# Kernel optimization log

Measured on AMD Instinct MI355X. Metric: run time of the kernel, lower is better.

## Reference

```python
import jax, jax.numpy as jnp
import numpy as np

B, C, H, W = 8, 256, 128, 128
CQ = C // 8


def setup_inputs() -> dict:
    key = jax.random.key(0)
    ks = jax.random.split(key, 8)
    s = 1.0 / np.sqrt(C)
    return {
        "x": jax.random.normal(ks[0], (B, C, H, W), dtype=jnp.float32),
        "wq": jax.random.normal(ks[1], (CQ, C), dtype=jnp.float32) * s,
        "bq": jax.random.normal(ks[2], (CQ,), dtype=jnp.float32) * 0.01,
        "wk": jax.random.normal(ks[3], (CQ, C), dtype=jnp.float32) * s,
        "bk": jax.random.normal(ks[4], (CQ,), dtype=jnp.float32) * 0.01,
        "wv": jax.random.normal(ks[5], (C, C), dtype=jnp.float32) * s,
        "bv": jax.random.normal(ks[6], (C,), dtype=jnp.float32) * 0.01,
        "gamma": jax.random.normal(ks[7], (1,), dtype=jnp.float32) * 0.1,
    }


def reference(x, wq, bq, wk, bk, wv, bv, gamma):
    b, c, h, w = x.shape
    # 1x1 convs == channel matmuls
    q = jnp.einsum("oc,bchw->bohw", wq, x) + bq[None, :, None, None]  # [B,Cq,H,W]
    k = jnp.einsum("oc,bchw->bohw", wk, x) + bk[None, :, None, None]  # [B,Cq,H,W]
    v = jnp.einsum("oc,bchw->bohw", wv, x) + bv[None, :, None, None]  # [B,C,H,W]

    # column (height) scores: energy_H[b,i,w,j] = <k[:, i, w], q[:, j, w]>, -inf on i==j
    e_h = jnp.einsum("bciw,bcjw->biwj", k, q)  # [B,H,W,H]
    diag = jnp.eye(h, dtype=bool)[:, None, :]  # [H,1,H] -> masks i==j
    e_h = jnp.where(diag[None], -jnp.inf, e_h)

    # row (width) scores: energy_W[b,h,i,j] = <k[:, h, i], q[:, h, j]>
    e_w = jnp.einsum("bchi,bchj->bhij", k, q)  # [B,H,W,W]

    # joint softmax over concatenated H+W scores (axis 3), as in the torch code
    att = jax.nn.softmax(jnp.concatenate([e_h, e_w], axis=3), axis=3)
    a_h, a_w = att[..., :h], att[..., h:]

    out_h = jnp.einsum("bciw,biwj->bcjw", v, a_h)  # aggregate along column
    out_w = jnp.einsum("bchi,bhij->bchj", v, a_w)  # aggregate along row
    return gamma * (out_h + out_w) + x
```

## Files before the change

### kernel.cpp

```cpp
#include <hip/hip_runtime.h>
#include <math.h>

#define C_   256
#define CQ_  32
#define H_   128
#define W_   128
#define HW_  (H_ * W_)
#define OC_  320

typedef __attribute__((ext_vector_type(8))) short  s8v;
typedef __attribute__((ext_vector_type(4))) float  f4v;
typedef __attribute__((ext_vector_type(8))) unsigned short u8v;
typedef __attribute__((ext_vector_type(4))) unsigned short u4v;

__device__ inline unsigned short f2bf(float f) {
    unsigned int u = __float_as_uint(f);
    unsigned int r = (u + 0x7fffu + ((u >> 16) & 1u)) >> 16;
    return (unsigned short)r;
}
__device__ inline float bfu(unsigned short u) {
    return __uint_as_float((unsigned int)u << 16);
}

__global__ __launch_bounds__(256) void k_wconv(
    const float* __restrict__ wq, const float* __restrict__ wk,
    const float* __restrict__ wv, unsigned short* __restrict__ Wb)
{
    int idx4 = blockIdx.x * 256 + threadIdx.x;
    int e = idx4 * 4;
    int oc = e >> 8, k = e & 255;
    const float* src;
    if (oc < 32)      src = wq + (size_t)oc * C_ + k;
    else if (oc < 64) src = wk + (size_t)(oc - 32) * C_ + k;
    else              src = wv + (size_t)(oc - 64) * C_ + k;
    float4 v = *(const float4*)src;
    u4v o;
    o[0] = f2bf(v.x); o[1] = f2bf(v.y); o[2] = f2bf(v.z); o[3] = f2bf(v.w);
    *(u4v*)(Wb + e) = o;
}

__global__ __launch_bounds__(256) void k_qkv(
    const float* __restrict__ x, const unsigned short* __restrict__ Wb,
    const float* __restrict__ bq, const float* __restrict__ bk,
    const float* __restrict__ bv,
    unsigned short* __restrict__ qkv, int b0)
{
    __shared__ __align__(16) unsigned short Wl[64][264];
    __shared__ __align__(16) unsigned int   Xp[32 * 132];
    const int t = threadIdx.x;
    const int lane = t & 63;
    const int wave = t >> 6;
    const int n0 = blockIdx.x * 128;
    const int ocblk = blockIdx.y * 64;
    const int bb = blockIdx.z;
    const float* xb = x + (size_t)(b0 + bb) * C_ * HW_;

    const int lg = lane >> 4;
    const int ll = lane & 15;
    const int n_w = wave * 32;

    const int kp8 = t >> 5;
    const int n4  = (t & 31) * 4;
    float4 ra[4], rb[4];

    #pragma unroll
    for (int p = 0; p < 4; ++p) {
        int krow = (p * 8 + kp8) * 2;
        ra[p] = *(const float4*)(xb + (size_t)krow * HW_ + n0 + n4);
        rb[p] = *(const float4*)(xb + (size_t)(krow + 1) * HW_ + n0 + n4);
    }

    #pragma unroll
    for (int q = 0; q < 8; ++q) {
        int chunk = t + q * 256;
        int row = chunk >> 5;
        int col = (chunk & 31) * 8;
        u8v w = *(const u8v*)(Wb + (size_t)(ocblk + row) * C_ + col);
        *(u8v*)&Wl[row][col] = w;
    }

    f4v acc[4][2];
    #pragma unroll
    for (int mr = 0; mr < 4; ++mr)
        #pragma unroll
        for (int nr = 0; nr < 2; ++nr)
            acc[mr][nr] = (f4v){0.f, 0.f, 0.f, 0.f};

    #pragma unroll
    for (int kc = 0; kc < 4; ++kc) {
        __syncthreads();
        #pragma unroll
        for (int p = 0; p < 4; ++p) {
            uint4 d;
            const float* af  = (const float*)&ra[p];
            const float* bf_ = (const float*)&rb[p];
            #pragma unroll
            for (int i = 0; i < 4; ++i) {
                unsigned int lo = (__float_as_uint(af[i])  + 0x8000u) >> 16;
                unsigned int hi = (__float_as_uint(bf_[i]) + 0x8000u) & 0xffff0000u;
                ((unsigned int*)&d)[i] = hi | lo;
            }
            *(uint4*)&Xp[(p * 8 + kp8) * 132 + n4] = d;
        }
        __syncthreads();
        if (kc < 3) {
            #pragma unroll
            for (int p = 0; p < 4; ++p) {
                int krow = (kc + 1) * 64 + (p * 8 + kp8) * 2;
                ra[p] = *(const float4*)(xb + (size_t)krow * HW_ + n0 + n4);
                rb[p] = *(const float4*)(xb + (size_t)(krow + 1) * HW_ + n0 + n4);
            }
        }
        #pragma unroll
        for (int ks = 0; ks < 2; ++ks) {
            s8v afr[4];
            #pragma unroll
            for (int mr = 0; mr < 4; ++mr)
                afr[mr] = *(const s8v*)&Wl[mr * 16 + ll][(kc * 2 + ks) * 32 + lg * 8];
            #pragma unroll
            for (int nr = 0; nr < 2; ++nr) {
                int4 bd;
                #pragma unroll
                for (int e2 = 0; e2 < 4; ++e2)
                    ((int*)&bd)[e2] =
                        Xp[(ks * 16 + lg * 4 + e2) * 132 + n_w + nr * 16 + ll];
                s8v bfr = *(s8v*)&bd;
                #pragma unroll
                for (int mr = 0; mr < 4; ++mr)
                    acc[mr][nr] = __builtin_amdgcn_mfma_f32_16x16x32_bf16(
                        afr[mr], bfr, acc[mr][nr], 0, 0, 0);
            }
        }
    }

    #pragma unroll
    for (int mr = 0; mr < 4; ++mr) {
        float bias[4];
        #pragma unroll
        for (int r = 0; r < 4; ++r) {
            int oc = ocblk + mr * 16 + lg * 4 + r;
            if (oc < 32)      bias[r] = bq[oc];
            else if (oc < 64) bias[r] = bk[oc - 32];
            else              bias[r] = bv[oc - 64];
        }
        #pragma unroll
        for (int nr = 0; nr < 2; ++nr) {
            int n = n0 + n_w + nr * 16 + ll;
            #pragma unroll
            for (int r = 0; r < 4; ++r) {
                int oc = ocblk + mr * 16 + lg * 4 + r;
                qkv[((size_t)bb * OC_ + oc) * HW_ + n] = f2bf(acc[mr][nr][r] + bias[r]);
            }
        }
    }
}

__global__ __launch_bounds__(256) void k_transpose_qkv(
    const unsigned short* __restrict__ qkv, unsigned short* __restrict__ qkv_t)
{
    __shared__ unsigned short tile[32][34];
    const int bb = blockIdx.z;
    const int oc = blockIdx.y;
    const int th = (blockIdx.x & 3) * 32;
    const int tw = (blockIdx.x >> 2) * 32;
    const unsigned short* src = qkv + ((size_t)bb * OC_ + oc) * HW_;
    #pragma unroll
    for (int r = 0; r < 4; ++r) {
        int h = threadIdx.y * 4 + r;
        tile[h][threadIdx.x] = src[(size_t)(th + h) * W_ + tw + threadIdx.x];
    }
    __syncthreads();
    unsigned short* dst = qkv_t + (size_t)bb * W_ * OC_ * H_;
    #pragma unroll
    for (int r = 0; r < 4; ++r) {
        int wl = threadIdx.y * 4 + r;
        dst[((size_t)(tw + wl) * OC_ + oc) * H_ + th + threadIdx.x] = tile[threadIdx.x][wl];
    }
}

__device__ inline void stage_KQ(const unsigned short* base, int cstride,
                                unsigned int* Ktp, unsigned int* Qp, int t)
{
    {
        int i = t & 127, half = t >> 7, c0 = half * 16;
        unsigned int kr[16];
        #pragma unroll
        for (int cc = 0; cc < 16; ++cc)
            kr[cc] = base[(size_t)(32 + c0 + cc) * cstride + i];
        uint4 d0, d1;
        #pragma unroll
        for (int e2 = 0; e2 < 4; ++e2)
            ((unsigned int*)&d0)[e2] = kr[2 * e2] | (kr[2 * e2 + 1] << 16);
        #pragma unroll
        for (int e2 = 0; e2 < 4; ++e2)
            ((unsigned int*)&d1)[e2] = kr[8 + 2 * e2] | (kr[9 + 2 * e2] << 16);
        *(uint4*)&Ktp[i * 20 + half * 8]     = d0;
        *(uint4*)&Ktp[i * 20 + half * 8 + 4] = d1;
    }
    {
        int c2 = t >> 4, j8 = (t & 15) * 8;
        u8v qa = *(const u8v*)(base + (size_t)(2 * c2) * cstride + j8);
        u8v qb = *(const u8v*)(base + (size_t)(2 * c2 + 1) * cstride + j8);
        uint4 e0, e1;
        #pragma unroll
        for (int e = 0; e < 4; ++e)
            ((unsigned int*)&e0)[e] =
                (unsigned int)qa[e] | ((unsigned int)qb[e] << 16);
        #pragma unroll
        for (int e = 0; e < 4; ++e)
            ((unsigned int*)&e1)[e] =
                (unsigned int)qa[4 + e] | ((unsigned int)qb[4 + e] << 16);
        *(uint4*)&Qp[c2 * 132 + j8]     = e0;
        *(uint4*)&Qp[c2 * 132 + j8 + 4] = e1;
    }
}

__device__ inline f4v eqk_mfma(const unsigned int* Ktp, const unsigned int* Qp,
                               int mr, int j, int lg, int ll)
{
    s8v afr = *(const s8v*)&Ktp[(mr * 16 + ll) * 20 + lg * 4];
    int4 bd;
    #pragma unroll
    for (int e2 = 0; e2 < 4; ++e2)
        ((int*)&bd)[e2] = Qp[(lg * 4 + e2) * 132 + j];
    s8v bfr = *(s8v*)&bd;
    return __builtin_amdgcn_mfma_f32_16x16x32_bf16(
        afr, bfr, (f4v){0.f, 0.f, 0.f, 0.f}, 0, 0, 0);
}

__global__ __launch_bounds__(256) void k_stats_h(
    const unsigned short* __restrict__ qkv_t,
    float* __restrict__ mh, float* __restrict__ sh)
{
    __shared__ __align__(16) unsigned int Ktp[128 * 20];
    __shared__ __align__(16) unsigned int Qp[16 * 132];
    const int t = threadIdx.x;
    const int beta = blockIdx.x;
    const int bb = blockIdx.y;
    const unsigned short* base = qkv_t + ((size_t)bb * W_ + beta) * OC_ * H_;
    stage_KQ(base, H_, Ktp, Qp, t);
    __syncthreads();

    const int lane = t & 63;
    const int wv = t >> 6;
    const int lg = lane >> 4;
    const int ll = lane & 15;

    #pragma unroll
    for (int ml = 0; ml < 2; ++ml) {
        const int mr = wv * 2 + ml;
        const int i0 = mr * 16 + lg * 4;
        f4v ef[8];
        #pragma unroll
        for (int nt = 0; nt < 8; ++nt) {
            f4v e = eqk_mfma(Ktp, Qp, mr, nt * 16 + ll, lg, ll);
            int j = nt * 16 + ll;
            #pragma unroll
            for (int r = 0; r < 4; ++r)
                if (i0 + r == j) e[r] = -INFINITY;
            ef[nt] = e;
        }
        #pragma unroll
        for (int r = 0; r < 4; ++r) {
            float mm = -INFINITY;
            #pragma unroll
            for (int nt = 0; nt < 8; ++nt) mm = fmaxf(mm, ef[nt][r]);
            #pragma unroll
            for (int s = 1; s < 16; s <<= 1) mm = fmaxf(mm, __shfl_xor(mm, s));
            float ss = 0.f;
            #pragma unroll
            for (int nt = 0; nt < 8; ++nt) ss += __expf(ef[nt][r] - mm);
            #pragma unroll
            for (int s = 1; s < 16; s <<= 1) ss += __shfl_xor(ss, s);
            if (ll == 0) {
                int i = i0 + r;
                mh[((size_t)bb * H_ + i) * W_ + beta] = mm;
                sh[((size_t)bb * H_ + i) * W_ + beta] = ss;
            }
        }
    }
}

__global__ __launch_bounds__(256) void k_stats_w(
    const unsigned short* __restrict__ qkv,
    float* __restrict__ mw, float* __restrict__ sw)
{
    __shared__ __align__(16) unsigned int Ktp[128 * 20];
    __shared__ __align__(16) unsigned int Qp[16 * 132];
    const int t = threadIdx.x;
    const int alpha = blockIdx.x;
    const int bb = blockIdx.y;
    const unsigned short* base = qkv + (size_t)bb * OC_ * HW_ + (size_t)alpha * W_;
    stage_KQ(base, HW_, Ktp, Qp, t);
    __syncthreads();

    const int lane = t & 63;
    const int wv = t >> 6;
    const int lg = lane >> 4;
    const int ll = lane & 15;

    #pragma unroll
    for (int ml = 0; ml < 2; ++ml) {
        const int mr = wv * 2 + ml;
        const int i0 = mr * 16 + lg * 4;
        f4v ef[8];
        #pragma unroll
        for (int nt = 0; nt < 8; ++nt)
            ef[nt] = eqk_mfma(Ktp, Qp, mr, nt * 16 + ll, lg, ll);
        #pragma unroll
        for (int r = 0; r < 4; ++r) {
            float mm = -INFINITY;
            #pragma unroll
            for (int nt = 0; nt < 8; ++nt) mm = fmaxf(mm, ef[nt][r]);
            #pragma unroll
            for (int s = 1; s < 16; s <<= 1) mm = fmaxf(mm, __shfl_xor(mm, s));
            float ss = 0.f;
            #pragma unroll
            for (int nt = 0; nt < 8; ++nt) ss += __expf(ef[nt][r] - mm);
            #pragma unroll
            for (int s = 1; s < 16; s <<= 1) ss += __shfl_xor(ss, s);
            if (ll == 0) {
                int i = i0 + r;
                mw[((size_t)bb * H_ + alpha) * W_ + i] = mm;
                sw[((size_t)bb * H_ + alpha) * W_ + i] = ss;
            }
        }
    }
}

__global__ __launch_bounds__(256) void k_prep(
    const float* __restrict__ mh, const float* __restrict__ sh,
    const float* __restrict__ mw, const float* __restrict__ sw,
    float* __restrict__ mc, float* __restrict__ dv,
    float* __restrict__ mct, float* __restrict__ dvt, int n)
{
    int idx = blockIdx.x * 256 + threadIdx.x;
    if (idx >= n) return;
    float m1 = mh[idx], s1 = sh[idx], m2 = mw[idx], s2 = sw[idx];
    float m = fmaxf(m1, m2);
    float d = 1.f / (s1 * __expf(m1 - m) + s2 * __expf(m2 - m));
    mc[idx] = m; dv[idx] = d;
    int q = idx & (W_ - 1);
    int p = (idx >> 7) & (H_ - 1);
    int b = idx >> 14;
    size_t tid = ((size_t)b * W_ + q) * H_ + p;
    mct[tid] = m; dvt[tid] = d;
}

__global__ __launch_bounds__(256) void k_outh(
    const unsigned short* __restrict__ qkv_t,
    const float* __restrict__ mct, const float* __restrict__ dvt,
    unsigned short* __restrict__ oh_t)
{
    __shared__ __align__(16) unsigned short Pt[128 * 128];
    __shared__ __align__(16) unsigned char  Ubuf[18688];
    __shared__ float mloc[128], dloc[128];
    unsigned int* Ktp = (unsigned int*)Ubuf;
    unsigned int* Qp  = (unsigned int*)(Ubuf + 10240);
    unsigned short* Vl = (unsigned short*)Ubuf;

    const int t = threadIdx.x;
    const int beta = blockIdx.x;
    const int bb = blockIdx.y;
    const unsigned short* base = qkv_t + ((size_t)bb * W_ + beta) * OC_ * H_;

    if (t < 128) {
        size_t sidx = ((size_t)bb * W_ + beta) * H_ + t;
        mloc[t] = mct[sidx];
        dloc[t] = dvt[sidx];
    }
    stage_KQ(base, H_, Ktp, Qp, t);
    __syncthreads();

    const int lane = t & 63;
    const int wv = t >> 6;
    const int lg = lane >> 4;
    const int ll = lane & 15;
    const int jq0 = wv * 32;

    #pragma unroll
    for (int mr = 0; mr < 8; ++mr) {
        const int i0 = mr * 16 + lg * 4;
        float mi[4], di[4];
        #pragma unroll
        for (int r = 0; r < 4; ++r) { mi[r] = mloc[i0 + r]; di[r] = dloc[i0 + r]; }
        #pragma unroll
        for (int nt = 0; nt < 2; ++nt) {
            int j = jq0 + nt * 16 + ll;
            f4v e = eqk_mfma(Ktp, Qp, mr, j, lg, ll);
            float p0 = (i0     == j) ? 0.f : __expf(e[0] - mi[0]) * di[0];
            float p1 = (i0 + 1 == j) ? 0.f : __expf(e[1] - mi[1]) * di[1];
            float p2 = (i0 + 2 == j) ? 0.f : __expf(e[2] - mi[2]) * di[2];
            float p3 = (i0 + 3 == j) ? 0.f : __expf(e[3] - mi[3]) * di[3];
            uint2 wd;
            wd.x = f2bf(p0) | ((unsigned int)f2bf(p1) << 16);
            wd.y = f2bf(p2) | ((unsigned int)f2bf(p3) << 16);
            int sidx = (j * 128 + i0) ^ ((j & 7) << 3);
            *(uint2*)&Pt[sidx] = wd;
        }
    }

    unsigned short* outbase = oh_t + ((size_t)bb * W_ + beta) * C_ * H_;

    for (int ch = 0; ch < 4; ++ch) {
        __syncthreads();
        const unsigned short* vsrc = base + (size_t)(64 + ch * 64) * H_;
        #pragma unroll
        for (int f = t; f < 1024; f += 256) {
            int c = f >> 4, i0 = (f & 15) * 8;
            u8v v = *(const u8v*)(vsrc + (size_t)c * H_ + i0);
            *(u8v*)&Vl[(c * 128 + i0) ^ ((c & 7) << 3)] = v;
        }
        __syncthreads();

        f4v acc[8];
        #pragma unroll
        for (int nt = 0; nt < 8; ++nt) acc[nt] = (f4v){0.f, 0.f, 0.f, 0.f};

        #pragma unroll
        for (int kk = 0; kk < 4; ++kk) {
            int crow = wv * 16 + ll;
            s8v afr = *(const s8v*)&Vl[(crow * 128 + kk * 32 + lg * 8) ^ ((crow & 7) << 3)];
            #pragma unroll
            for (int nt = 0; nt < 8; ++nt) {
                int j = nt * 16 + ll;
                s8v bfr = *(const s8v*)&Pt[(j * 128 + kk * 32 + lg * 8) ^ ((j & 7) << 3)];
                acc[nt] = __builtin_amdgcn_mfma_f32_16x16x32_bf16(afr, bfr, acc[nt], 0, 0, 0);
            }
        }
        #pragma unroll
        for (int nt = 0; nt < 8; ++nt) {
            int j = nt * 16 + ll;
            #pragma unroll
            for (int r = 0; r < 4; ++r) {
                int c = ch * 64 + wv * 16 + lg * 4 + r;
                outbase[(size_t)c * H_ + j] = f2bf(acc[nt][r]);
            }
        }
    }
}

__global__ __launch_bounds__(256) void k_outw(
    const unsigned short* __restrict__ qkv,
    const float* __restrict__ mc, const float* __restrict__ dv_,
    unsigned short* __restrict__ ow)
{
    __shared__ __align__(16) unsigned short Pt[128 * 128];
    __shared__ __align__(16) unsigned char  Ubuf[18688];
    __shared__ float mloc[128], dloc[128];
    unsigned int* Ktp = (unsigned int*)Ubuf;
    unsigned int* Qp  = (unsigned int*)(Ubuf + 10240);
    unsigned short* Vl = (unsigned short*)Ubuf;

    const int t = threadIdx.x;
    const int alpha = blockIdx.x;
    const int bb = blockIdx.y;
    const unsigned short* base = qkv + (size_t)bb * OC_ * HW_ + (size_t)alpha * W_;

    if (t < 128) {
        size_t sidx = ((size_t)bb * H_ + alpha) * W_ + t;
        mloc[t] = mc[sidx];
        dloc[t] = dv_[sidx];
    }
    stage_KQ(base, HW_, Ktp, Qp, t);
    __syncthreads();

    const int lane = t & 63;
    const int wv = t >> 6;
    const int lg = lane >> 4;
    const int ll = lane & 15;
    const int jq0 = wv * 32;

    #pragma unroll
    for (int mr = 0; mr < 8; ++mr) {
        const int i0 = mr * 16 + lg * 4;
        float mi[4], di[4];
        #pragma unroll
        for (int r = 0; r < 4; ++r) { mi[r] = mloc[i0 + r]; di[r] = dloc[i0 + r]; }
        #pragma unroll
        for (int nt = 0; nt < 2; ++nt) {
            int j = jq0 + nt * 16 + ll;
            f4v e = eqk_mfma(Ktp, Qp, mr, j, lg, ll);
            float p0 = __expf(e[0] - mi[0]) * di[0];
            float p1 = __expf(e[1] - mi[1]) * di[1];
            float p2 = __expf(e[2] - mi[2]) * di[2];
            float p3 = __expf(e[3] - mi[3]) * di[3];
            uint2 wd;
            wd.x = f2bf(p0) | ((unsigned int)f2bf(p1) << 16);
            wd.y = f2bf(p2) | ((unsigned int)f2bf(p3) << 16);
            int sidx = (j * 128 + i0) ^ ((j & 7) << 3);
            *(uint2*)&Pt[sidx] = wd;
        }
    }

    unsigned short* obase = ow + (size_t)bb * C_ * HW_ + (size_t)alpha * W_;

    for (int ch = 0; ch < 4; ++ch) {
        __syncthreads();
        const unsigned short* vsrc = base + (size_t)(64 + ch * 64) * HW_;
        #pragma unroll
        for (int f = t; f < 1024; f += 256) {
            int c = f >> 4, i0 = (f & 15) * 8;
            u8v v = *(const u8v*)(vsrc + (size_t)c * HW_ + i0);
            *(u8v*)&Vl[(c * 128 + i0) ^ ((c & 7) << 3)] = v;
        }
        __syncthreads();

        f4v acc[8];
        #pragma unroll
        for (int nt = 0; nt < 8; ++nt) acc[nt] = (f4v){0.f, 0.f, 0.f, 0.f};

        #pragma unroll
        for (int kk = 0; kk < 4; ++kk) {
            int crow = wv * 16 + ll;
            s8v afr = *(const s8v*)&Vl[(crow * 128 + kk * 32 + lg * 8) ^ ((crow & 7) << 3)];
            #pragma unroll
            for (int nt = 0; nt < 8; ++nt) {
                int j = nt * 16 + ll;
                s8v bfr = *(const s8v*)&Pt[(j * 128 + kk * 32 + lg * 8) ^ ((j & 7) << 3)];
                acc[nt] = __builtin_amdgcn_mfma_f32_16x16x32_bf16(afr, bfr, acc[nt], 0, 0, 0);
            }
        }
        #pragma unroll
        for (int nt = 0; nt < 8; ++nt) {
            int j = nt * 16 + ll;
            #pragma unroll
            for (int r = 0; r < 4; ++r) {
                int c = ch * 64 + wv * 16 + lg * 4 + r;
                obase[(size_t)c * HW_ + j] = f2bf(acc[nt][r]);
            }
        }
    }
}

__global__ __launch_bounds__(256) void k_combine(
    const unsigned short* __restrict__ oh_t, const unsigned short* __restrict__ ow,
    const float* __restrict__ x, const float* __restrict__ gamma_p,
    float* __restrict__ out, int b0)
{
    __shared__ float tile[32][33];
    const int bb = blockIdx.z;
    const int c = blockIdx.y;
    const int th = (blockIdx.x & 3) * 32;
    const int tw = (blockIdx.x >> 2) * 32;
    const float gamma = gamma_p[0];
    const unsigned short* src = oh_t + (size_t)bb * W_ * C_ * H_;
    #pragma unroll
    for (int r = 0; r < 4; ++r) {
        int wl = threadIdx.y * 4 + r;
        tile[wl][threadIdx.x] =
            bfu(src[((size_t)(tw + wl) * C_ + c) * H_ + th + threadIdx.x]);
    }
    __syncthreads();
    const size_t pbase = ((size_t)bb * C_ + c) * HW_;
    const size_t gbase = ((size_t)(b0 + bb) * C_ + c) * HW_;
    #pragma unroll
    for (int r = 0; r < 4; ++r) {
        int hl = threadIdx.y * 4 + r;
        size_t idx = (size_t)(th + hl) * W_ + tw + threadIdx.x;
        float owv = bfu(ow[pbase + idx]);
        out[gbase + idx] = x[gbase + idx] + gamma * (owv + tile[threadIdx.x][hl]);
    }
}

extern "C" void kernel_launch(void* const* d_in, const int* in_sizes, int n_in,
                              void* d_out, int out_size, void* d_ws, size_t ws_size,
                              hipStream_t stream)
{
    (void)in_sizes; (void)n_in; (void)out_size;
    const float* x  = (const float*)d_in[0];
    const float* wq = (const float*)d_in[1];
    const float* bq = (const float*)d_in[2];
    const float* wk = (const float*)d_in[3];
    const float* bk = (const float*)d_in[4];
    const float* wv = (const float*)d_in[5];
    const float* bv = (const float*)d_in[6];
    const float* gm = (const float*)d_in[7];
    float* out = (float*)d_out;

    const size_t e_qkv  = (size_t)OC_ * HW_;
    const size_t e_out  = (size_t)C_ * HW_;
    const size_t e_stat = (size_t)HW_;
    const size_t perb_bytes = (e_qkv * 2 + e_out * 2) * 2 + e_stat * 8 * 4;
    const size_t wb_bytes = (size_t)OC_ * C_ * 2;
    int nbcap = (int)((ws_size - wb_bytes) / perb_bytes);
    if (nbcap > 8) nbcap = 8;
    if (nbcap < 1) nbcap = 1;

    unsigned short* Wb    = (unsigned short*)d_ws;
    unsigned short* qkv   = Wb    + (size_t)OC_ * C_;
    unsigned short* qkv_t = qkv   + e_qkv * nbcap;
    unsigned short* oh    = qkv_t + e_qkv * nbcap;
    unsigned short* ow    = oh    + e_out * nbcap;
    float* mh  = (float*)(ow + e_out * nbcap);
    float* sh  = mh  + e_stat * nbcap;
    float* mw  = sh  + e_stat * nbcap;
    float* sw  = mw  + e_stat * nbcap;
    float* mc  = sw  + e_stat * nbcap;
    float* dv  = mc  + e_stat * nbcap;
    float* mct = dv  + e_stat * nbcap;
    float* dvt = mct + e_stat * nbcap;

    k_wconv<<<dim3(80), 256, 0, stream>>>(wq, wk, wv, Wb);

    for (int b0 = 0; b0 < 8; b0 += nbcap) {
        int nb = 8 - b0 < nbcap ? 8 - b0 : nbcap;
        k_qkv<<<dim3(HW_ / 128, 5, nb), 256, 0, stream>>>(
            x, Wb, bq, bk, bv, qkv, b0);
        k_transpose_qkv<<<dim3(16, OC_, nb), dim3(32, 8), 0, stream>>>(qkv, qkv_t);
        k_stats_h<<<dim3(W_, nb), 256, 0, stream>>>(qkv_t, mh, sh);
        k_stats_w<<<dim3(H_, nb), 256, 0, stream>>>(qkv, mw, sw);
        int nstat = nb * HW_;
        k_prep<<<dim3((nstat + 255) / 256), 256, 0, stream>>>(
            mh, sh, mw, sw, mc, dv, mct, dvt, nstat);
        k_outh<<<dim3(W_, nb), 256, 0, stream>>>(qkv_t, mct, dvt, oh);
        k_outw<<<dim3(H_, nb), 256, 0, stream>>>(qkv, mc, dv, ow);
        k_combine<<<dim3(16, C_, nb), dim3(32, 8), 0, stream>>>(
            oh, ow, x, gm, out, b0);
    }
}
```

Baseline: 308.6 us.

## Widen QKV projection tile to 160 output channels and prefetch V chunks

The QKV projection kernel now computes 160 output channels per block instead of 64, so each x tile is read from global memory and converted to bf16 twice rather than five times. Weights are streamed per 64-wide K chunk through registers instead of being staged in full. Separately, the outh and outw kernels prefetch the next V chunk into registers while the MFMAs for the current chunk run. The cost is much higher register pressure (20 accumulator vectors per thread) and a smaller grid for the projection kernel, which may reduce occupancy.

```diff
diff --git a/kernel.cpp b/kernel.cpp
--- a/kernel.cpp
+++ b/kernel.cpp
@@ -45,13 +45,13 @@
     const float* __restrict__ bv,
     unsigned short* __restrict__ qkv, int b0)
 {
-    __shared__ __align__(16) unsigned short Wl[64][264];
+    __shared__ __align__(16) unsigned short Wl[160][72];
     __shared__ __align__(16) unsigned int   Xp[32 * 132];
     const int t = threadIdx.x;
     const int lane = t & 63;
     const int wave = t >> 6;
     const int n0 = blockIdx.x * 128;
-    const int ocblk = blockIdx.y * 64;
+    const int ocblk = blockIdx.y * 160;
     const int bb = blockIdx.z;
     const float* xb = x + (size_t)(b0 + bb) * C_ * HW_;
 
@@ -61,7 +61,10 @@
 
     const int kp8 = t >> 5;
     const int n4  = (t & 31) * 4;
+    const int wrow = t >> 3;
+    const int wcg  = (t & 7) * 8;
     float4 ra[4], rb[4];
+    u8v wreg[5];
 
     #pragma unroll
     for (int p = 0; p < 4; ++p) {
@@ -69,19 +72,13 @@
         ra[p] = *(const float4*)(xb + (size_t)krow * HW_ + n0 + n4);
         rb[p] = *(const float4*)(xb + (size_t)(krow + 1) * HW_ + n0 + n4);
     }
-
-    #pragma unroll
-    for (int q = 0; q < 8; ++q) {
-        int chunk = t + q * 256;
-        int row = chunk >> 5;
-        int col = (chunk & 31) * 8;
-        u8v w = *(const u8v*)(Wb + (size_t)(ocblk + row) * C_ + col);
-        *(u8v*)&Wl[row][col] = w;
-    }
-
-    f4v acc[4][2];
-    #pragma unroll
-    for (int mr = 0; mr < 4; ++mr)
+    #pragma unroll
+    for (int q = 0; q < 5; ++q)
+        wreg[q] = *(const u8v*)(Wb + (size_t)(ocblk + wrow + q * 32) * C_ + wcg);
+
+    f4v acc[10][2];
+    #pragma unroll
+    for (int mr = 0; mr < 10; ++mr)
         #pragma unroll
         for (int nr = 0; nr < 2; ++nr)
             acc[mr][nr] = (f4v){0.f, 0.f, 0.f, 0.f};
@@ -102,6 +99,9 @@
             }
             *(uint4*)&Xp[(p * 8 + kp8) * 132 + n4] = d;
         }
+        #pragma unroll
+        for (int q = 0; q < 5; ++q)
+            *(u8v*)&Wl[wrow + q * 32][wcg] = wreg[q];
         __syncthreads();
         if (kc < 3) {
             #pragma unroll
@@ -110,13 +110,14 @@
                 ra[p] = *(const float4*)(xb + (size_t)krow * HW_ + n0 + n4);
                 rb[p] = *(const float4*)(xb + (size_t)(krow + 1) * HW_ + n0 + n4);
             }
+            #pragma unroll
+            for (int q = 0; q < 5; ++q)
+                wreg[q] = *(const u8v*)(
+                    Wb + (size_t)(ocblk + wrow + q * 32) * C_ + (kc + 1) * 64 + wcg);
         }
         #pragma unroll
         for (int ks = 0; ks < 2; ++ks) {
-            s8v afr[4];
-            #pragma unroll
-            for (int mr = 0; mr < 4; ++mr)
-                afr[mr] = *(const s8v*)&Wl[mr * 16 + ll][(kc * 2 + ks) * 32 + lg * 8];
+            s8v bfr[2];
             #pragma unroll
             for (int nr = 0; nr < 2; ++nr) {
                 int4 bd;
@@ -124,17 +125,21 @@
                 for (int e2 = 0; e2 < 4; ++e2)
                     ((int*)&bd)[e2] =
                         Xp[(ks * 16 + lg * 4 + e2) * 132 + n_w + nr * 16 + ll];
-                s8v bfr = *(s8v*)&bd;
+                bfr[nr] = *(s8v*)&bd;
+            }
+            #pragma unroll
+            for (int mr = 0; mr < 10; ++mr) {
+                s8v afr = *(const s8v*)&Wl[mr * 16 + ll][ks * 32 + lg * 8];
                 #pragma unroll
-                for (int mr = 0; mr < 4; ++mr)
+                for (int nr = 0; nr < 2; ++nr)
                     acc[mr][nr] = __builtin_amdgcn_mfma_f32_16x16x32_bf16(
-                        afr[mr], bfr, acc[mr][nr], 0, 0, 0);
-            }
-        }
-    }
-
-    #pragma unroll
-    for (int mr = 0; mr < 4; ++mr) {
+                        afr, bfr[nr], acc[mr][nr], 0, 0, 0);
+            }
+        }
+    }
+
+    #pragma unroll
+    for (int mr = 0; mr < 10; ++mr) {
         float bias[4];
         #pragma unroll
         for (int r = 0; r < 4; ++r) {
@@ -370,6 +375,16 @@
         dloc[t] = dvt[sidx];
     }
     stage_KQ(base, H_, Ktp, Qp, t);
+
+    const int vc  = t >> 4;
+    const int vi0 = (t & 15) * 8;
+    u8v vreg[4];
+    {
+        const unsigned short* vsrc = base + (size_t)64 * H_;
+        #pragma unroll
+        for (int q = 0; q < 4; ++q)
+            vreg[q] = *(const u8v*)(vsrc + (size_t)(vc + q * 16) * H_ + vi0);
+    }
     __syncthreads();
 
     const int lane = t & 63;
@@ -404,14 +419,18 @@
 
     for (int ch = 0; ch < 4; ++ch) {
         __syncthreads();
-        const unsigned short* vsrc = base + (size_t)(64 + ch * 64) * H_;
-        #pragma unroll
-        for (int f = t; f < 1024; f += 256) {
-            int c = f >> 4, i0 = (f & 15) * 8;
-            u8v v = *(const u8v*)(vsrc + (size_t)c * H_ + i0);
-            *(u8v*)&Vl[(c * 128 + i0) ^ ((c & 7) << 3)] = v;
+        #pragma unroll
+        for (int q = 0; q < 4; ++q) {
+            int c = vc + q * 16;
+            *(u8v*)&Vl[(c * 128 + vi0) ^ ((c & 7) << 3)] = vreg[q];
         }
         __syncthreads();
+        if (ch < 3) {
+            const unsigned short* vsrc = base + (size_t)(64 + (ch + 1) * 64) * H_;
+            #pragma unroll
+            for (int q = 0; q < 4; ++q)
+                vreg[q] = *(const u8v*)(vsrc + (size_t)(vc + q * 16) * H_ + vi0);
+        }
 
         f4v acc[8];
         #pragma unroll
@@ -463,6 +482,16 @@
         dloc[t] = dv_[sidx];
     }
     stage_KQ(base, HW_, Ktp, Qp, t);
+
+    const int vc  = t >> 4;
+    const int vi0 = (t & 15) * 8;
+    u8v vreg[4];
+    {
+        const unsigned short* vsrc = base + (size_t)64 * HW_;
+        #pragma unroll
+        for (int q = 0; q < 4; ++q)
+            vreg[q] = *(const u8v*)(vsrc + (size_t)(vc + q * 16) * HW_ + vi0);
+    }
     __syncthreads();
 
     const int lane = t & 63;
@@ -497,14 +526,18 @@
 
     for (int ch = 0; ch < 4; ++ch) {
         __syncthreads();
-        const unsigned short* vsrc = base + (size_t)(64 + ch * 64) * HW_;
-        #pragma unroll
-        for (int f = t; f < 1024; f += 256) {
-            int c = f >> 4, i0 = (f & 15) * 8;
-            u8v v = *(const u8v*)(vsrc + (size_t)c * HW_ + i0);
-            *(u8v*)&Vl[(c * 128 + i0) ^ ((c & 7) << 3)] = v;
+        #pragma unroll
+        for (int q = 0; q < 4; ++q) {
+            int c = vc + q * 16;
+            *(u8v*)&Vl[(c * 128 + vi0) ^ ((c & 7) << 3)] = vreg[q];
         }
         __syncthreads();
+        if (ch < 3) {
+            const unsigned short* vsrc = base + (size_t)(64 + (ch + 1) * 64) * HW_;
+            #pragma unroll
+            for (int q = 0; q < 4; ++q)
+                vreg[q] = *(const u8v*)(vsrc + (size_t)(vc + q * 16) * HW_ + vi0);
+        }
 
         f4v acc[8];
         #pragma unroll
@@ -605,7 +638,7 @@
 
     for (int b0 = 0; b0 < 8; b0 += nbcap) {
         int nb = 8 - b0 < nbcap ? 8 - b0 : nbcap;
-        k_qkv<<<dim3(HW_ / 128, 5, nb), 256, 0, stream>>>(
+        k_qkv<<<dim3(HW_ / 128, 2, nb), 256, 0, stream>>>(
             x, Wb, bq, bk, bv, qkv, b0);
         k_transpose_qkv<<<dim3(16, OC_, nb), dim3(32, 8), 0, stream>>>(qkv, qkv_t);
         k_stats_h<<<dim3(W_, nb), 256, 0, stream>>>(qkv_t, mh, sh);
```

Result: no change. 304.8 us (-1.2%).
